# Kernel tuning notes

Measured on AMD Instinct MI355X. Metric: run time of the kernel, lower is better.

The kernel has to match this reference:

```python
import jax, jax.numpy as jnp
import numpy as np

K = 3          # kernel_size
STRIDE = 1
PAD = 1
DIL = 1


def conv2d(x, w, b, stride=STRIDE, pad=PAD, dil=DIL):
    y = jax.lax.conv_general_dilated(
        x, w, window_strides=(stride, stride),
        padding=((pad, pad), (pad, pad)), rhs_dilation=(dil, dil),
        dimension_numbers=('NCHW', 'OIHW', 'NCHW'))
    if b is not None:
        y = y + b[None, :, None, None]
    return y


def bilinear_gather(x, py, px):
    """Zero-padded bilinear sampling.
    x: [B,C,H,W]; py,px: [B,K2,Ho,Wo] float coords. Returns [B,C,K2,Ho,Wo].
    Matches torchvision deform_conv2d: out-of-range corners contribute zero."""
    B, C, H, W = x.shape
    y0 = jnp.floor(py)
    x0 = jnp.floor(px)
    wy1 = py - y0
    wx1 = px - x0
    wy0 = 1.0 - wy1
    wx0 = 1.0 - wx1
    xf = x.reshape(B, C, H * W)

    def corner(yi, xi, wgt):
        valid = (yi >= 0) & (yi < H) & (xi >= 0) & (xi < W)
        yc = jnp.clip(yi, 0, H - 1).astype(jnp.int32)
        xc = jnp.clip(xi, 0, W - 1).astype(jnp.int32)
        idx = (yc * W + xc).reshape(B, 1, -1)            # [B,1,K2*Ho*Wo]
        v = jnp.take_along_axis(xf, idx, axis=2)         # [B,C,K2*Ho*Wo]
        v = v.reshape(B, C, *yi.shape[1:])               # [B,C,K2,Ho,Wo]
        w = (wgt * valid.astype(x.dtype))[:, None]       # [B,1,K2,Ho,Wo]
        return v * w

    return (corner(y0, x0, wy0 * wx0) + corner(y0, x0 + 1, wy0 * wx1)
            + corner(y0 + 1, x0, wy1 * wx0) + corner(y0 + 1, x0 + 1, wy1 * wx1))


def reference(x, w_offset, b_offset, w_mask, b_mask, w_deform):
    B, C, H, W = x.shape
    K2 = K * K
    offset = conv2d(x, w_offset, b_offset)               # [B,2*K2,Ho,Wo]
    mask = jax.nn.sigmoid(conv2d(x, w_mask, b_mask))     # [B,K2,Ho,Wo]
    Ho, Wo = offset.shape[2], offset.shape[3]

    off = offset.reshape(B, K2, 2, Ho, Wo)
    dy, dx = off[:, :, 0], off[:, :, 1]                  # [B,K2,Ho,Wo]

    ky = (jnp.arange(K2) // K).astype(x.dtype) * DIL     # kernel tap row offsets
    kx = (jnp.arange(K2) % K).astype(x.dtype) * DIL
    base_y = (jnp.arange(Ho) * STRIDE - PAD).astype(x.dtype)
    base_x = (jnp.arange(Wo) * STRIDE - PAD).astype(x.dtype)
    py = dy + base_y[None, None, :, None] + ky[None, :, None, None]
    px = dx + base_x[None, None, None, :] + kx[None, :, None, None]

    val = bilinear_gather(x, py, px)                     # [B,C,K2,Ho,Wo]
    val = val * mask[:, None]                            # modulation

    w = w_deform.reshape(w_deform.shape[0], C, K2)       # [Cout,Cin,K2]
    return jnp.einsum('bckhw,ock->bohw', val, w)


def setup_inputs() -> dict:
    key = jax.random.key(0)
    k = jax.random.split(key, 6)
    B, Cin, Cout, H, W = 2, 64, 64, 224, 224
    x = jax.random.normal(k[0], (B, Cin, H, W), dtype=jnp.float32)
    # source zero-inits offset/mask convs; use small random weights to exercise
    # fractional, scattered sampling coordinates.
    w_offset = jax.random.normal(k[1], (2 * K * K, Cin, K, K), dtype=jnp.float32) * 0.01
    b_offset = jnp.zeros((2 * K * K,), dtype=jnp.float32)
    w_mask = jax.random.normal(k[2], (K * K, Cin, K, K), dtype=jnp.float32) * 0.01
    b_mask = jnp.zeros((K * K,), dtype=jnp.float32)
    w_deform = jax.random.normal(k[3], (Cout, Cin, K, K), dtype=jnp.float32) * (1.0 / np.sqrt(Cin * K * K))
    return {"x": x, "w_offset": w_offset, "b_offset": b_offset,
            "w_mask": w_mask, "b_mask": b_mask, "w_deform": w_deform}
```

## Files before the change

kernel.cpp:

```cpp
#include <hip/hip_runtime.h>
#include <math.h>

constexpr int B    = 2;
constexpr int C    = 64;
constexpr int H    = 224;
constexpr int W    = 224;
constexpr int Hp   = 226;
constexpr int Wp   = 226;
constexpr int K2   = 9;
constexpr int OCO  = 18;
constexpr int OM   = 27;
constexpr int COUT = 64;
constexpr int HW   = H * W;
constexpr int NPIX = B * HW;
constexpr int CK   = C * K2;

typedef short  bf16x8 __attribute__((ext_vector_type(8)));
typedef float  f32x4  __attribute__((ext_vector_type(4)));

__device__ inline unsigned short f2bf(float f) {
    union { float f; unsigned u; } v; v.f = f;
    unsigned r = v.u + 0x7FFF + ((v.u >> 16) & 1);
    return (unsigned short)(r >> 16);
}
__device__ inline unsigned pack2(float a, float b) {
    return (unsigned)f2bf(a) | ((unsigned)f2bf(b) << 16);
}

__global__ __launch_bounds__(256) void k_padT(const float* __restrict__ x,
                                              float* __restrict__ xp) {
    __shared__ float tile[32][33];
    const int b   = blockIdx.z;
    const int hw0 = blockIdx.x * 32;
    const int c0  = blockIdx.y * 32;
    const int tx  = threadIdx.x;
    const int ty  = threadIdx.y;
    const float* xb  = x  + (size_t)b * C * HW;
    float*       xpb = xp + (size_t)b * Hp * Wp * C;
#pragma unroll
    for (int j = 0; j < 4; ++j) {
        int c = c0 + ty + j * 8;
        tile[ty + j * 8][tx] = xb[(size_t)c * HW + hw0 + tx];
    }
    __syncthreads();
#pragma unroll
    for (int j = 0; j < 4; ++j) {
        int hw = hw0 + ty + j * 8;
        int y  = hw / W;
        int xx = hw % W;
        xpb[((size_t)(y + 1) * Wp + (xx + 1)) * C + c0 + tx] = tile[tx][ty + j * 8];
    }
}

__global__ void k_wA(const float* __restrict__ wd, unsigned short* __restrict__ wA) {
    int i = blockIdx.x * 256 + threadIdx.x;
    if (i >= COUT * CK) return;
    int o  = i / CK;
    int kc = i % CK;
    int k  = kc >> 6;
    int c  = kc & 63;
    wA[i] = f2bf(wd[((size_t)o * C + c) * 9 + k]);
}

__global__ void k_womA(const float* __restrict__ w_off,
                       const float* __restrict__ w_msk,
                       const float* __restrict__ b_off,
                       const float* __restrict__ b_msk,
                       unsigned short* __restrict__ womA,
                       float* __restrict__ biasv) {
    int i = blockIdx.x * 256 + threadIdx.x;
    if (i < 32) biasv[i] = (i < OCO) ? b_off[i] : (i < OM) ? b_msk[i - OCO] : 0.f;
    if (i >= 32 * CK) return;
    int oc = i / CK;
    int kc = i % CK;
    int k  = kc >> 6;
    int c  = kc & 63;
    float v = (oc < OCO) ? w_off[((size_t)oc * C + c) * 9 + k]
            : (oc < OM)  ? w_msk[((size_t)(oc - OCO) * C + c) * 9 + k]
                         : 0.f;
    womA[i] = f2bf(v);
}

__global__ __launch_bounds__(256) void k_convom(const float* __restrict__ xp,
                                                const unsigned short* __restrict__ womA,
                                                const float* __restrict__ biasv,
                                                float* __restrict__ offmask) {
    __shared__ __align__(16) unsigned short imcol[64 * CK];
    const int tid  = threadIdx.x;
    const int lane = tid & 63;
    const int wv   = tid >> 6;
    const int q    = lane >> 4;
    const int l15  = lane & 15;
    const int pix0 = blockIdx.x * 64;
    const int bb   = pix0 / HW;
    const float* xb = xp + (size_t)bb * Hp * Wp * C;

    const int c0 = l15 * 4;
    for (int pi = 0; pi < 4; ++pi) {
        const int p_local = wv * 16 + pi * 4 + q;
        const int pix = pix0 + p_local;
        const int hw  = pix - bb * HW;
        const int y   = hw / W;
        const int xx  = hw % W;
#pragma unroll
        for (int k = 0; k < 9; ++k) {
            const int ky = k / 3, kx = k % 3;
            const float4 v = *reinterpret_cast<const float4*>(
                xb + ((size_t)(y + ky) * Wp + (xx + kx)) * C + c0);
            int byte = p_local * (CK * 2) + k * 128 + l15 * 8;
            byte ^= (p_local & 7) << 4;
            *reinterpret_cast<uint2*>(reinterpret_cast<char*>(imcol) + byte) =
                make_uint2(pack2(v.x, v.y), pack2(v.z, v.w));
        }
    }
    __syncthreads();

    f32x4 acc0 = {0.f, 0.f, 0.f, 0.f}, acc1 = {0.f, 0.f, 0.f, 0.f};
    const unsigned short* a0 = womA + (size_t)l15 * CK;
    const unsigned short* a1 = womA + (size_t)(16 + l15) * CK;
    const int row = wv * 16 + l15;
#pragma unroll 3
    for (int ks = 0; ks < 18; ++ks) {
        int byte = row * (CK * 2) + ks * 64 + q * 16;
        byte ^= (row & 7) << 4;
        const bf16x8 bfv = *reinterpret_cast<const bf16x8*>(
            reinterpret_cast<const char*>(imcol) + byte);
        const bf16x8 af0 = *reinterpret_cast<const bf16x8*>(a0 + ks * 32 + q * 8);
        const bf16x8 af1 = *reinterpret_cast<const bf16x8*>(a1 + ks * 32 + q * 8);
        acc0 = __builtin_amdgcn_mfma_f32_16x16x32_bf16(af0, bfv, acc0, 0, 0, 0);
        acc1 = __builtin_amdgcn_mfma_f32_16x16x32_bf16(af1, bfv, acc1, 0, 0, 0);
    }

    const int  pixn = pix0 + wv * 16 + l15;
    float* om = offmask + (size_t)pixn * OM;
#pragma unroll
    for (int r = 0; r < 4; ++r) {
        const int oc = q * 4 + r;
        om[oc] = acc0[r] + biasv[oc];
    }
#pragma unroll
    for (int r = 0; r < 4; ++r) {
        const int oc = 16 + q * 4 + r;
        if (oc < OM) {
            float v = acc1[r] + biasv[oc];
            om[oc] = (oc < OCO) ? v : 1.0f / (1.0f + __expf(-v));
        }
    }
}

constexpr int PPB = 64;

__global__ __launch_bounds__(256) void k_deform(const float* __restrict__ xp,
                                                const float* __restrict__ offmask,
                                                const unsigned short* __restrict__ wA,
                                                float* __restrict__ out) {
    __shared__ __align__(16) unsigned short valT[64 * CK];
    const int tid  = threadIdx.x;
    const int lane = tid & 63;
    const int wv   = tid >> 6;
    const int q    = lane >> 4;
    const int l15  = lane & 15;
    const int pix0 = blockIdx.x * PPB;
    const int bb   = pix0 / HW;
    const float* xb = xp + (size_t)bb * Hp * Wp * C;

    const int c0 = l15 * 4;
    for (int pi = 0; pi < 4; ++pi) {
        const int p_local = wv * 16 + pi * 4 + q;
        const int pix = pix0 + p_local;
        const int hw  = pix - bb * HW;
        const int ho  = hw / W;
        const int wo  = hw % W;
        const float* om = offmask + (size_t)pix * OM;
#pragma unroll 3
        for (int k = 0; k < 9; ++k) {
            const float dy = om[2 * k];
            const float dx = om[2 * k + 1];
            const float m  = om[OCO + k];
            const float py = dy + (float)(ho - 1 + k / 3);
            const float px = dx + (float)(wo - 1 + k % 3);
            const float fy = floorf(py), fx = floorf(px);
            const int   y0 = (int)fy,   x0 = (int)fx;
            const float wy1 = py - fy,  wx1 = px - fx;
            const float wy0 = 1.f - wy1, wx0 = 1.f - wx1;
            const bool iy0 = (y0 >= 0) & (y0 < H);
            const bool iy1 = (y0 + 1 >= 0) & (y0 + 1 < H);
            const bool ix0 = (x0 >= 0) & (x0 < W);
            const bool ix1 = (x0 + 1 >= 0) & (x0 + 1 < W);
            const float w00 = wy0 * wx0 * ((iy0 & ix0) ? 1.f : 0.f);
            const float w01 = wy0 * wx1 * ((iy0 & ix1) ? 1.f : 0.f);
            const float w10 = wy1 * wx0 * ((iy1 & ix0) ? 1.f : 0.f);
            const float w11 = wy1 * wx1 * ((iy1 & ix1) ? 1.f : 0.f);
            const int ya = min(max(y0 + 1, 0), Hp - 1);
            const int yb = min(max(y0 + 2, 0), Hp - 1);
            const int xa = min(max(x0 + 1, 0), Wp - 1);
            const int xc = min(max(x0 + 2, 0), Wp - 1);
            const float4 v00 = *reinterpret_cast<const float4*>(xb + ((size_t)ya * Wp + xa) * C + c0);
            const float4 v01 = *reinterpret_cast<const float4*>(xb + ((size_t)ya * Wp + xc) * C + c0);
            const float4 v10 = *reinterpret_cast<const float4*>(xb + ((size_t)yb * Wp + xa) * C + c0);
            const float4 v11 = *reinterpret_cast<const float4*>(xb + ((size_t)yb * Wp + xc) * C + c0);
            const float s0 = m * (w00 * v00.x + w01 * v01.x + w10 * v10.x + w11 * v11.x);
            const float s1 = m * (w00 * v00.y + w01 * v01.y + w10 * v10.y + w11 * v11.y);
            const float s2 = m * (w00 * v00.z + w01 * v01.z + w10 * v10.z + w11 * v11.z);
            const float s3 = m * (w00 * v00.w + w01 * v01.w + w10 * v10.w + w11 * v11.w);
            int byte = p_local * (CK * 2) + k * 128 + l15 * 8;
            byte ^= (p_local & 7) << 4;
            *reinterpret_cast<uint2*>(reinterpret_cast<char*>(valT) + byte) =
                make_uint2(pack2(s0, s1), pack2(s2, s3));
        }
    }
    __syncthreads();

    f32x4 acc[4] = {{0.f,0.f,0.f,0.f},{0.f,0.f,0.f,0.f},{0.f,0.f,0.f,0.f},{0.f,0.f,0.f,0.f}};
    const unsigned short* wrow = wA + (size_t)(wv * 16 + l15) * CK;
#pragma unroll 3
    for (int ks = 0; ks < 18; ++ks) {
        const bf16x8 af = *reinterpret_cast<const bf16x8*>(wrow + ks * 32 + q * 8);
#pragma unroll
        for (int nt = 0; nt < 4; ++nt) {
            const int row = nt * 16 + l15;
            int byte = row * (CK * 2) + ks * 64 + q * 16;
            byte ^= (row & 7) << 4;
            const bf16x8 bfv = *reinterpret_cast<const bf16x8*>(
                reinterpret_cast<const char*>(valT) + byte);
            acc[nt] = __builtin_amdgcn_mfma_f32_16x16x32_bf16(af, bfv, acc[nt], 0, 0, 0);
        }
    }

    const int o0 = wv * 16 + q * 4;
#pragma unroll
    for (int nt = 0; nt < 4; ++nt) {
        const int pixn = pix0 + nt * 16 + l15;
        const int hw   = pixn - bb * HW;
#pragma unroll
        for (int r = 0; r < 4; ++r)
            out[((size_t)bb * COUT + o0 + r) * HW + hw] = acc[nt][r];
    }
}

extern "C" void kernel_launch(void* const* d_in, const int* in_sizes, int n_in,
                              void* d_out, int out_size, void* d_ws, size_t ws_size,
                              hipStream_t stream) {
    const float* x     = (const float*)d_in[0];
    const float* w_off = (const float*)d_in[1];
    const float* b_off = (const float*)d_in[2];
    const float* w_msk = (const float*)d_in[3];
    const float* b_msk = (const float*)d_in[4];
    const float* w_def = (const float*)d_in[5];
    float* out = (float*)d_out;

    float* ws      = (float*)d_ws;
    float* xpadT   = ws;
    float* offmask = xpadT + (size_t)B * Hp * Wp * C;
    float* biasv   = offmask + (size_t)NPIX * OM;
    unsigned short* wA   = (unsigned short*)(biasv + 32);
    unsigned short* womA = wA + (size_t)COUT * CK;

    hipMemsetAsync(xpadT, 0, (size_t)B * Hp * Wp * C * sizeof(float), stream);

    k_padT<<<dim3(HW / 32, C / 32, B), dim3(32, 8), 0, stream>>>(x, xpadT);
    k_wA<<<(COUT * CK + 255) / 256, 256, 0, stream>>>(w_def, wA);
    k_womA<<<(32 * CK + 255) / 256, 256, 0, stream>>>(w_off, w_msk, b_off, b_msk,
                                                      womA, biasv);
    k_convom<<<NPIX / 64, 256, 0, stream>>>(xpadT, womA, biasv, offmask);
    k_deform<<<NPIX / PPB, 256, 0, stream>>>(xpadT, offmask, wA, out);
}
```

Baseline: 219.0 us.

## Precompute bilinear gather offsets and weights in conv kernel, zero only pad border

Moves the bilinear coordinate, clamping, validity and mask-weight computation from the deform kernel into the epilogue of the offset/mask conv kernel. That epilogue now writes per-tap int4 corner offsets and float4 premultiplied weights, so the deform kernel only loads those and does the gathers. The full-buffer memset of the padded input is replaced with a small kernel that zeroes only the border cells. Bf16 packing switches to the library converter. The trade is a larger intermediate table (32 bytes per pixel-tap versus 27 floats per pixel) plus an extra LDS staging pass and syncs in the conv kernel, in exchange for removing redundant per-lane coordinate math in the deform gather.

```diff
diff --git a/kernel.cpp b/kernel.cpp
--- a/kernel.cpp
+++ b/kernel.cpp
@@ -1,4 +1,5 @@
 #include <hip/hip_runtime.h>
+#include <hip/hip_bf16.h>
 #include <math.h>
 
 constexpr int B    = 2;
@@ -23,8 +24,10 @@
     unsigned r = v.u + 0x7FFF + ((v.u >> 16) & 1);
     return (unsigned short)(r >> 16);
 }
-__device__ inline unsigned pack2(float a, float b) {
-    return (unsigned)f2bf(a) | ((unsigned)f2bf(b) << 16);
+__device__ inline unsigned cvtpk(float a, float b) {
+    __hip_bfloat162 h = __float22bfloat162_rn(make_float2(a, b));
+    union { __hip_bfloat162 h; unsigned u; } cv; cv.h = h;
+    return cv.u;
 }
 
 __global__ __launch_bounds__(256) void k_padT(const float* __restrict__ x,
@@ -50,6 +53,21 @@
         int xx = hw % W;
         xpb[((size_t)(y + 1) * Wp + (xx + 1)) * C + c0 + tx] = tile[tx][ty + j * 8];
     }
+}
+
+__global__ void k_border(float* __restrict__ xp) {
+    int i = blockIdx.x * 256 + threadIdx.x;
+    if (i >= B * 900 * 16) return;
+    int chunk = i & 15;
+    int cell  = (i >> 4) % 900;
+    int b     = (i >> 4) / 900;
+    int y, x;
+    if      (cell < 226) { y = 0;              x = cell; }
+    else if (cell < 452) { y = Hp - 1;         x = cell - 226; }
+    else if (cell < 676) { y = cell - 452 + 1; x = 0; }
+    else                 { y = cell - 676 + 1; x = Wp - 1; }
+    float4 z = make_float4(0.f, 0.f, 0.f, 0.f);
+    *reinterpret_cast<float4*>(xp + ((size_t)b * Hp * Wp + y * Wp + x) * C + chunk * 4) = z;
 }
 
 __global__ void k_wA(const float* __restrict__ wd, unsigned short* __restrict__ wA) {
@@ -84,7 +102,8 @@
 __global__ __launch_bounds__(256) void k_convom(const float* __restrict__ xp,
                                                 const unsigned short* __restrict__ womA,
                                                 const float* __restrict__ biasv,
-                                                float* __restrict__ offmask) {
+                                                int4* __restrict__ gtabO,
+                                                float4* __restrict__ gtabW) {
     __shared__ __align__(16) unsigned short imcol[64 * CK];
     const int tid  = threadIdx.x;
     const int lane = tid & 63;
@@ -102,15 +121,15 @@
         const int hw  = pix - bb * HW;
         const int y   = hw / W;
         const int xx  = hw % W;
+        int wbase = p_local * (CK * 2) + l15 * 8;
+        wbase ^= (p_local & 7) << 4;
 #pragma unroll
         for (int k = 0; k < 9; ++k) {
             const int ky = k / 3, kx = k % 3;
             const float4 v = *reinterpret_cast<const float4*>(
                 xb + ((size_t)(y + ky) * Wp + (xx + kx)) * C + c0);
-            int byte = p_local * (CK * 2) + k * 128 + l15 * 8;
-            byte ^= (p_local & 7) << 4;
-            *reinterpret_cast<uint2*>(reinterpret_cast<char*>(imcol) + byte) =
-                make_uint2(pack2(v.x, v.y), pack2(v.z, v.w));
+            *reinterpret_cast<uint2*>(reinterpret_cast<char*>(imcol) + wbase + k * 128) =
+                make_uint2(cvtpk(v.x, v.y), cvtpk(v.z, v.w));
         }
     }
     __syncthreads();
@@ -131,27 +150,67 @@
         acc1 = __builtin_amdgcn_mfma_f32_16x16x32_bf16(af1, bfv, acc1, 0, 0, 0);
     }
 
-    const int  pixn = pix0 + wv * 16 + l15;
-    float* om = offmask + (size_t)pixn * OM;
-#pragma unroll
-    for (int r = 0; r < 4; ++r) {
-        const int oc = q * 4 + r;
-        om[oc] = acc0[r] + biasv[oc];
-    }
-#pragma unroll
-    for (int r = 0; r < 4; ++r) {
-        const int oc = 16 + q * 4 + r;
-        if (oc < OM) {
-            float v = acc1[r] + biasv[oc];
-            om[oc] = (oc < OCO) ? v : 1.0f / (1.0f + __expf(-v));
-        }
+    __syncthreads();
+    float* som = reinterpret_cast<float*>(imcol);
+    {
+        const int p = wv * 16 + l15;
+#pragma unroll
+        for (int r = 0; r < 4; ++r) {
+            const int oc = q * 4 + r;
+            som[p * 28 + oc] = acc0[r] + biasv[oc];
+        }
+#pragma unroll
+        for (int r = 0; r < 4; ++r) {
+            const int oc = 16 + q * 4 + r;
+            if (oc < OM) {
+                float v = acc1[r] + biasv[oc];
+                som[p * 28 + oc] = (oc < OCO) ? v : 1.0f / (1.0f + __expf(-v));
+            }
+        }
+    }
+    __syncthreads();
+
+    for (int e = tid; e < 64 * 9; e += 256) {
+        const int p  = e / 9;
+        const int k  = e - p * 9;
+        const int pix = pix0 + p;
+        const int hw  = pix - bb * HW;
+        const int ho  = hw / W;
+        const int wo  = hw - ho * W;
+        const int ky  = k / 3, kx = k - (k / 3) * 3;
+        const float dy = som[p * 28 + 2 * k];
+        const float dx = som[p * 28 + 2 * k + 1];
+        const float m  = som[p * 28 + OCO + k];
+        const float py = dy + (float)(ho + ky - 1);
+        const float px = dx + (float)(wo + kx - 1);
+        const float fy = floorf(py), fx = floorf(px);
+        const int   y0 = (int)fy,   x0 = (int)fx;
+        const float wy1 = py - fy,  wx1 = px - fx;
+        const float wy0 = 1.f - wy1, wx0 = 1.f - wx1;
+        const bool iy0 = (y0 >= 0) & (y0 < H);
+        const bool iy1 = (y0 + 1 >= 0) & (y0 + 1 < H);
+        const bool ix0 = (x0 >= 0) & (x0 < W);
+        const bool ix1 = (x0 + 1 >= 0) & (x0 + 1 < W);
+        const int ya = min(max(y0 + 1, 0), Hp - 1);
+        const int yb = min(max(y0 + 2, 0), Hp - 1);
+        const int xa = min(max(x0 + 1, 0), Wp - 1);
+        const int xc = min(max(x0 + 2, 0), Wp - 1);
+        const int rA = ya * Wp, rB = yb * Wp;
+        gtabO[(size_t)pix * 9 + k] = make_int4((rA + xa) * C, (rA + xc) * C,
+                                               (rB + xa) * C, (rB + xc) * C);
+        gtabW[(size_t)pix * 9 + k] = make_float4(
+            wy0 * wx0 * m * ((iy0 & ix0) ? 1.f : 0.f),
+            wy0 * wx1 * m * ((iy0 & ix1) ? 1.f : 0.f),
+            wy1 * wx0 * m * ((iy1 & ix0) ? 1.f : 0.f),
+            wy1 * wx1 * m * ((iy1 & ix1) ? 1.f : 0.f));
     }
 }
 
 constexpr int PPB = 64;
 
 __global__ __launch_bounds__(256) void k_deform(const float* __restrict__ xp,
-                                                const float* __restrict__ offmask,
+                                                const int4* __restrict__ gtabO,
+                                                const float4* __restrict__ gtabW,
                                                 const unsigned short* __restrict__ wA,
                                                 float* __restrict__ out) {
     __shared__ __align__(16) unsigned short valT[64 * CK];
@@ -168,45 +227,24 @@
     for (int pi = 0; pi < 4; ++pi) {
         const int p_local = wv * 16 + pi * 4 + q;
         const int pix = pix0 + p_local;
-        const int hw  = pix - bb * HW;
-        const int ho  = hw / W;
-        const int wo  = hw % W;
-        const float* om = offmask + (size_t)pix * OM;
-#pragma unroll 3
+        const int4*   gO = gtabO + (size_t)pix * 9;
+        const float4* gW = gtabW + (size_t)pix * 9;
+        int wbase = p_local * (CK * 2) + l15 * 8;
+        wbase ^= (p_local & 7) << 4;
+#pragma unroll
         for (int k = 0; k < 9; ++k) {
-            const float dy = om[2 * k];
-            const float dx = om[2 * k + 1];
-            const float m  = om[OCO + k];
-            const float py = dy + (float)(ho - 1 + k / 3);
-            const float px = dx + (float)(wo - 1 + k % 3);
-            const float fy = floorf(py), fx = floorf(px);
-            const int   y0 = (int)fy,   x0 = (int)fx;
-            const float wy1 = py - fy,  wx1 = px - fx;
-            const float wy0 = 1.f - wy1, wx0 = 1.f - wx1;
-            const bool iy0 = (y0 >= 0) & (y0 < H);
-            const bool iy1 = (y0 + 1 >= 0) & (y0 + 1 < H);
-            const bool ix0 = (x0 >= 0) & (x0 < W);
-            const bool ix1 = (x0 + 1 >= 0) & (x0 + 1 < W);
-            const float w00 = wy0 * wx0 * ((iy0 & ix0) ? 1.f : 0.f);
-            const float w01 = wy0 * wx1 * ((iy0 & ix1) ? 1.f : 0.f);
-            const float w10 = wy1 * wx0 * ((iy1 & ix0) ? 1.f : 0.f);
-            const float w11 = wy1 * wx1 * ((iy1 & ix1) ? 1.f : 0.f);
-            const int ya = min(max(y0 + 1, 0), Hp - 1);
-            const int yb = min(max(y0 + 2, 0), Hp - 1);
-            const int xa = min(max(x0 + 1, 0), Wp - 1);
-            const int xc = min(max(x0 + 2, 0), Wp - 1);
-            const float4 v00 = *reinterpret_cast<const float4*>(xb + ((size_t)ya * Wp + xa) * C + c0);
-            const float4 v01 = *reinterpret_cast<const float4*>(xb + ((size_t)ya * Wp + xc) * C + c0);
-            const float4 v10 = *reinterpret_cast<const float4*>(xb + ((size_t)yb * Wp + xa) * C + c0);
-            const float4 v11 = *reinterpret_cast<const float4*>(xb + ((size_t)yb * Wp + xc) * C + c0);
-            const float s0 = m * (w00 * v00.x + w01 * v01.x + w10 * v10.x + w11 * v11.x);
-            const float s1 = m * (w00 * v00.y + w01 * v01.y + w10 * v10.y + w11 * v11.y);
-            const float s2 = m * (w00 * v00.z + w01 * v01.z + w10 * v10.z + w11 * v11.z);
-            const float s3 = m * (w00 * v00.w + w01 * v01.w + w10 * v10.w + w11 * v11.w);
-            int byte = p_local * (CK * 2) + k * 128 + l15 * 8;
-            byte ^= (p_local & 7) << 4;
-            *reinterpret_cast<uint2*>(reinterpret_cast<char*>(valT) + byte) =
-                make_uint2(pack2(s0, s1), pack2(s2, s3));
+            const int4   o  = gO[k];
+            const float4 wt = gW[k];
+            const float4 v00 = *reinterpret_cast<const float4*>(xb + o.x + c0);
+            const float4 v01 = *reinterpret_cast<const float4*>(xb + o.y + c0);
+            const float4 v10 = *reinterpret_cast<const float4*>(xb + o.z + c0);
+            const float4 v11 = *reinterpret_cast<const float4*>(xb + o.w + c0);
+            const float s0 = wt.x * v00.x + wt.y * v01.x + wt.z * v10.x + wt.w * v11.x;
+            const float s1 = wt.x * v00.y + wt.y * v01.y + wt.z * v10.y + wt.w * v11.y;
+            const float s2 = wt.x * v00.z + wt.y * v01.z + wt.z * v10.z + wt.w * v11.z;
+            const float s3 = wt.x * v00.w + wt.y * v01.w + wt.z * v10.w + wt.w * v11.w;
+            *reinterpret_cast<uint2*>(reinterpret_cast<char*>(valT) + wbase + k * 128) =
+                make_uint2(cvtpk(s0, s1), cvtpk(s2, s3));
         }
     }
     __syncthreads();
@@ -249,19 +287,19 @@
     const float* w_def = (const float*)d_in[5];
     float* out = (float*)d_out;
 
-    float* ws      = (float*)d_ws;
-    float* xpadT   = ws;
-    float* offmask = xpadT + (size_t)B * Hp * Wp * C;
-    float* biasv   = offmask + (size_t)NPIX * OM;
+    float* ws    = (float*)d_ws;
+    float* xpadT = ws;
+    int4*   gtabO = (int4*)(xpadT + (size_t)B * Hp * Wp * C);
+    float4* gtabW = (float4*)(gtabO + (size_t)NPIX * 9);
+    float*  biasv = (float*)(gtabW + (size_t)NPIX * 9);
     unsigned short* wA   = (unsigned short*)(biasv + 32);
     unsigned short* womA = wA + (size_t)COUT * CK;
 
-    hipMemsetAsync(xpadT, 0, (size_t)B * Hp * Wp * C * sizeof(float), stream);
-
+    k_border<<<(B * 900 * 16 + 255) / 256, 256, 0, stream>>>(xpadT);
     k_padT<<<dim3(HW / 32, C / 32, B), dim3(32, 8), 0, stream>>>(x, xpadT);
     k_wA<<<(COUT * CK + 255) / 256, 256, 0, stream>>>(w_def, wA);
     k_womA<<<(32 * CK + 255) / 256, 256, 0, stream>>>(w_off, w_msk, b_off, b_msk,
                                                       womA, biasv);
-    k_convom<<<NPIX / 64, 256, 0, stream>>>(xpadT, womA, biasv, offmask);
-    k_deform<<<NPIX / PPB, 256, 0, stream>>>(xpadT, offmask, wA, out);
-}
+    k_convom<<<NPIX / 64, 256, 0, stream>>>(xpadT, womA, biasv, gtabO, gtabW);
+    k_deform<<<NPIX / PPB, 256, 0, stream>>>(xpadT, gtabO, gtabW, wA, out);
+}
```

After: 204.4 us. 1.07x faster.
